# Performance work log

Hardware: AMD Instinct MI355X
Metric: run time of the kernel (lower is better)

## Reference

```python
import jax, jax.numpy as jnp
import numpy as np

B, N, C, H, NC, P = 16, 577, 768, 12, 8, 576  # batch, seq(=patches+cls), dim, heads, curves, patches
D = C // H


def setup_inputs() -> dict:
    key = jax.random.key(0)
    ks = jax.random.split(key, 8)
    x = jax.random.normal(ks[0], (B, N, C), jnp.float32)
    qkv_w = jax.random.normal(ks[1], (C, 3 * C), jnp.float32) * 0.02
    proj_w = jax.random.normal(ks[2], (C, C), jnp.float32) * 0.02
    proj_b = jnp.zeros((C,), jnp.float32)
    # learned per-head decay logits; +3 so sigmoid ~0.95 (slow decay, realistic)
    ai_list = jax.random.normal(ks[3], (NC, H), jnp.float32) + 3.0
    mask_weights = jax.random.normal(ks[4], (NC,), jnp.float32) * 0.1 + 1.0 / NC
    normalize = 1.0 + 0.1 * jax.random.normal(ks[5], (H,), jnp.float32)
    # space-filling-curve inverse index permutations (one per curve)
    curve_inds = jnp.stack([
        jax.random.permutation(jax.random.fold_in(ks[6], c), P) for c in range(NC)
    ]).astype(jnp.int32)
    return dict(x=x, qkv_w=qkv_w, proj_w=proj_w, proj_b=proj_b,
                ai_list=ai_list, mask_weights=mask_weights,
                normalize=normalize, curve_inds=curve_inds)


def _build_mask(ai_list, mask_weights, curve_inds):
    # sigmoid(a)^|i-j| gathered by the curve permutation == sigmoid(a)^|ind_i - ind_j|
    a = jax.nn.sigmoid(ai_list)                                  # [NC,H]
    ci = curve_inds.astype(jnp.float32)                          # [NC,P]
    diff = jnp.abs(ci[:, :, None] - ci[:, None, :])              # [NC,P,P]
    Mc = a[:, :, None, None] ** diff[:, None, :, :]              # [NC,H,P,P]
    Mp = jnp.einsum('c,chpq->hpq', mask_weights, Mc)             # weighted sum over curves
    # cls-token row/col: each curve contributes ones -> sum of weights
    sw = jnp.sum(mask_weights)
    M = jnp.pad(Mp, ((0, 0), (1, 0), (1, 0)))                    # [H,N,N]
    M = M.at[:, 0, :].set(sw)
    M = M.at[:, :, 0].set(sw)
    return M


def reference(x, qkv_w, proj_w, proj_b, ai_list, mask_weights, normalize, curve_inds):
    qkv = (x @ qkv_w).reshape(B, N, 3, H, D)
    q = jnp.transpose(qkv[:, :, 0], (0, 2, 1, 3))                # [B,H,N,D]
    k = jnp.transpose(qkv[:, :, 1], (0, 2, 1, 3))
    v = jnp.transpose(qkv[:, :, 2], (0, 2, 1, 3))
    # NOTE: original overwrites self.scale with the bool `scale`=True -> multiply by 1
    attn = jnp.einsum('bhnd,bhmd->bhnm', q, k)                   # [B,H,N,N]
    M = _build_mask(ai_list, mask_weights, curve_inds)           # [H,N,N]
    attn = attn * M[None] * normalize[None, :, None, None]       # method='mul_v1'
    attn = jax.nn.softmax(attn, axis=-1)
    out = jnp.einsum('bhnm,bhmd->bhnd', attn, v)
    out = jnp.transpose(out, (0, 2, 1, 3)).reshape(B, N, C)
    return out @ proj_w + proj_b
```

## Files before the change

kernel.cpp:

```cpp
#include <hip/hip_runtime.h>


typedef _Float16 f16;
typedef _Float16 half8 __attribute__((ext_vector_type(8)));
typedef _Float16 half4 __attribute__((ext_vector_type(4)));
typedef float floatx4 __attribute__((ext_vector_type(4)));

#define DEVINL __device__ __forceinline__

#define Bb 16
#define NN 577
#define CC 768
#define HH 12
#define DD 64
#define MM (Bb * NN)
#define VTLD 584
#define MLD 580
#define CLD 136
#define TLD 264

DEVINL void async_copy16(void* lds, const void* g) {
  __builtin_amdgcn_global_load_lds(
      (const __attribute__((address_space(1))) void*)g,
      (__attribute__((address_space(3))) void*)lds, 16, 0, 0);
}

DEVINL half8 ld_swz(const f16* lds, int row, int chunk) {
  return *(const half8*)(lds + row * 64 + ((chunk ^ (row & 7)) << 3));
}

DEVINL int xcd_swizzle(int orig, int nwg) {
  int q = nwg >> 3, r = nwg & 7;
  int xcd = orig & 7, loc = orig >> 3;
  return (xcd < r ? xcd * (q + 1) : r * (q + 1) + (xcd - r) * q) + loc;
}

__global__ __launch_bounds__(256)
void prep_kernel(const float* __restrict__ x, const float* __restrict__ qkvw,
                 const float* __restrict__ pw, const float* __restrict__ ai,
                 const float* __restrict__ mw, const float* __restrict__ nrm,
                 const int* __restrict__ ci, f16* __restrict__ x_h,
                 f16* __restrict__ w_t, f16* __restrict__ pw_t,
                 float* __restrict__ Mb) {
  __shared__ float shm[32 * 33];
  const int bid = blockIdx.x;
  const int tid = threadIdx.x;
  if (bid < 6924) {
    int i = (bid * 256 + tid) * 4;
    float4 v = *(const float4*)(x + i);
    half4 o = {(f16)v.x, (f16)v.y, (f16)v.z, (f16)v.w};
    *(half4*)(x_h + i) = o;
  } else if (bid < 9228) {
    bool isq = bid < 8652;
    int b2 = bid - (isq ? 6924 : 8652);
    int N3 = isq ? 3 * CC : CC;
    const float* in = isq ? qkvw : pw;
    f16* out = isq ? w_t : pw_t;
    const int k0 = (b2 % 24) * 32, n0 = (b2 / 24) * 32;
    const int tx = tid & 31, ty = tid >> 5;
#pragma unroll
    for (int p = 0; p < 4; ++p)
      shm[(ty + p * 8) * 33 + tx] = in[(size_t)(k0 + ty + p * 8) * N3 + n0 + tx];
    __syncthreads();
#pragma unroll
    for (int p = 0; p < 4; ++p)
      out[(size_t)(n0 + ty + p * 8) * CC + k0 + tx] = (f16)shm[tx * 33 + ty + p * 8];
  } else {
    int b4 = bid - 9228;
    int i = b4 % NN, h = b4 / NN;
    float* la_s = shm; float* wv_s = shm + 8; float* cif = shm + 16;
    float* swn_s = shm + 24;
    if (tid < 8) {
      float av = ai[tid * 12 + h];
      float a = 1.f / (1.f + __expf(-av));
      la_s[tid] = __logf(a);
      wv_s[tid] = mw[tid];
      cif[tid] = (i > 0) ? (float)ci[tid * 576 + (i - 1)] : 0.f;
    }
    if (tid == 0) {
      float s = 0.f;
      for (int c = 0; c < 8; ++c) s += mw[c];
      swn_s[0] = s * nrm[h] * 1.44269504088896f;
    }
    __syncthreads();
    const float nr = nrm[h] * 1.44269504088896f;
    float* row = Mb + ((size_t)h * NN + i) * MLD;
    for (int j = tid; j < NN; j += 256) {
      float val;
      if (i == 0 || j == 0) {
        val = swn_s[0];
      } else {
        float acc = 0.f;
#pragma unroll
        for (int c = 0; c < 8; ++c) {
          float d = fabsf(cif[c] - (float)ci[c * 576 + (j - 1)]);
          acc += wv_s[c] * __expf(la_s[c] * d);
        }
        val = acc * nr;
      }
      row[j] = val;
    }
  }
}

DEVINL void gemm_mainloop(const f16* __restrict__ A, const f16* __restrict__ Bt,
                          int arow0, int brow0, int maxar,
                          f16* SMEM, floatx4 acc[4][4], int tid) {
  const int lane = tid & 63;
  const int wid = tid >> 6;
  const int wr = wid >> 1, wc = wid & 1;
  const int l15 = lane & 15, g = lane >> 4;
  const int r_ = tid >> 3, cp_ = tid & 7;
  const int lc_ = (cp_ ^ (r_ & 7)) << 3;

  auto stage = [&](f16* As, f16* Bs, int k0) {
#pragma unroll
    for (int q = 0; q < 4; ++q) {
      int r = q * 64 + r_;
      int ar = arow0 + r; if (ar > maxar) ar = maxar;
      async_copy16(As + (q * 512 + tid) * 8, A + (size_t)ar * CC + k0 + lc_);
    }
#pragma unroll
    for (int q = 0; q < 2; ++q) {
      int r = q * 64 + r_;
      async_copy16(Bs + (q * 512 + tid) * 8, Bt + (size_t)(brow0 + r) * CC + k0 + lc_);
    }
  };
  auto compute = [&](const f16* As, const f16* Bs) {
#pragma unroll
    for (int kk = 0; kk < 2; ++kk) {
      half8 af[4], bf[4];
#pragma unroll
      for (int mi = 0; mi < 4; ++mi) af[mi] = ld_swz(As, wr * 64 + mi * 16 + l15, kk * 4 + g);
#pragma unroll
      for (int ni = 0; ni < 4; ++ni) bf[ni] = ld_swz(Bs, wc * 64 + ni * 16 + l15, kk * 4 + g);
#pragma unroll
      for (int mi = 0; mi < 4; ++mi)
#pragma unroll
        for (int ni = 0; ni < 4; ++ni)
          acc[mi][ni] = __builtin_amdgcn_mfma_f32_16x16x32_f16(af[mi], bf[ni], acc[mi][ni], 0, 0, 0);
    }
  };

  const int nt = CC / 64;
  stage(SMEM, SMEM + 16384, 0);
#pragma unroll 1
  for (int t = 0; t < nt; ++t) {
    f16* cAs = (t & 1) ? SMEM + 24576 : SMEM;
    f16* cBs = (t & 1) ? SMEM + 40960 : SMEM + 16384;
    f16* nAs = (t & 1) ? SMEM : SMEM + 24576;
    f16* nBs = (t & 1) ? SMEM + 16384 : SMEM + 40960;
    if (t + 1 < nt) {
      stage(nAs, nBs, (t + 1) * 64);
      asm volatile("s_waitcnt vmcnt(6)" ::: "memory");
    } else {
      asm volatile("s_waitcnt vmcnt(0)" ::: "memory");
    }
    __builtin_amdgcn_s_barrier();
    __builtin_amdgcn_sched_barrier(0);
    compute(cAs, cBs);
    __builtin_amdgcn_s_barrier();
  }
}

__global__ __launch_bounds__(512, 2)
void gemm_qkv(const f16* __restrict__ A, const f16* __restrict__ Bt,
              f16* __restrict__ qb, f16* __restrict__ kb, f16* __restrict__ vt) {
  __shared__ __align__(16) f16 SMEM[49152];
  floatx4 acc[4][4] = {};
  const int nwg = 18 * 37;
  const int wgid = xcd_swizzle(blockIdx.y * gridDim.x + blockIdx.x, nwg);
  const int m0 = (wgid / 18) * 256, n0 = (wgid % 18) * 128;
  gemm_mainloop(A, Bt, m0, n0, MM - 1, SMEM, acc, threadIdx.x);
  const int tid = threadIdx.x, lane = tid & 63, wid = tid >> 6;
  const int wr = wid >> 1, wc = wid & 1, l15 = lane & 15, g = lane >> 4;
  const int t = n0 / CC;
  const int h0 = (n0 - t * CC) >> 6;
  if (t < 2) {
#pragma unroll
    for (int mi = 0; mi < 4; ++mi)
#pragma unroll
      for (int ni = 0; ni < 4; ++ni)
#pragma unroll
        for (int r = 0; r < 4; ++r)
          SMEM[(wr * 64 + mi * 16 + 4 * g + r) * CLD + wc * 64 + ni * 16 + l15] =
              (f16)acc[mi][ni][r];
    __syncthreads();
    f16* dst = (t == 0) ? qb : kb;
#pragma unroll
    for (int p = 0; p < 8; ++p) {
      int c = p * 512 + tid;
      int ml = c >> 4, n3c = (c & 15) << 3;
      int mg = m0 + ml;
      if (mg < MM) {
        int b = mg / NN, n = mg - b * NN;
        int h = h0 + (n3c >> 6), d0 = n3c & 63;
        half8 v = *(const half8*)(SMEM + ml * CLD + n3c);
        *(half8*)(dst + ((size_t)(b * HH + h) * NN + n) * DD + d0) = v;
      }
    }
  } else {
#pragma unroll
    for (int mi = 0; mi < 4; ++mi)
#pragma unroll
      for (int ni = 0; ni < 4; ++ni)
#pragma unroll
        for (int r = 0; r < 4; ++r)
          SMEM[(wc * 64 + ni * 16 + l15) * TLD + wr * 64 + mi * 16 + 4 * g + r] =
              (f16)acc[mi][ni][r];
    __syncthreads();
#pragma unroll
    for (int p = 0; p < 8; ++p) {
      int c = p * 512 + tid;
      int n3 = c >> 5, mc = (c & 31) << 3;
      int mg = m0 + mc;
      int h = h0 + (n3 >> 6), d = n3 & 63;
      half8 v = *(const half8*)(SMEM + n3 * TLD + mc);
      int b0 = mg / NN;
      if (mg + 7 < MM && (mg + 7) / NN == b0) {
        *(half8*)(vt + ((size_t)(b0 * HH + h) * DD + d) * VTLD + (mg - b0 * NN)) = v;
      } else {
#pragma unroll
        for (int e = 0; e < 8; ++e) {
          int m2 = mg + e;
          if (m2 < MM) {
            int b = m2 / NN;
            vt[((size_t)(b * HH + h) * DD + d) * VTLD + (m2 - b * NN)] = v[e];
          }
        }
      }
    }
  }
}

__global__ __launch_bounds__(512, 2)
void gemm_proj(const f16* __restrict__ A, const f16* __restrict__ Bt,
               const float* __restrict__ bias, float* __restrict__ out) {
  __shared__ __align__(16) f16 SMEM[49152];
  floatx4 acc[4][4] = {};
  const int nwg = 6 * 37;
  const int wgid = xcd_swizzle(blockIdx.y * gridDim.x + blockIdx.x, nwg);
  const int m0 = (wgid / 6) * 256, n0 = (wgid % 6) * 128;
  gemm_mainloop(A, Bt, m0, n0, MM - 1, SMEM, acc, threadIdx.x);
  const int lane = threadIdx.x & 63, wid = threadIdx.x >> 6;
  const int wr = wid >> 1, wc = wid & 1, l15 = lane & 15, g = lane >> 4;
#pragma unroll
  for (int mi = 0; mi < 4; ++mi)
#pragma unroll
    for (int ni = 0; ni < 4; ++ni)
#pragma unroll
      for (int r = 0; r < 4; ++r) {
        int m = m0 + wr * 64 + mi * 16 + 4 * g + r;
        if (m >= MM) continue;
        int n = n0 + wc * 64 + ni * 16 + l15;
        out[(size_t)m * CC + n] = acc[mi][ni][r] + bias[n];
      }
}

__global__ __launch_bounds__(512, 4)
void attn_kernel(const f16* __restrict__ qb, const f16* __restrict__ kb,
                 const f16* __restrict__ vt, const float* __restrict__ Mb,
                 f16* __restrict__ aout) {
  __shared__ f16 Ks[2][64 * 64];
  __shared__ f16 Vs[2][64 * 64];
  const int D0 = (blockIdx.z * gridDim.y + blockIdx.y) * gridDim.x + blockIdx.x;
  const int wgid = xcd_swizzle(D0, 5 * HH * Bb);
  const int it = wgid % 5;
  const int rem = wgid / 5;
  const int b = rem % Bb, h = rem / Bb;
  const int tid = threadIdx.x, lane = tid & 63, wid = tid >> 6;
  const int l15 = lane & 15, g = lane >> 4;
  const size_t bh = (size_t)b * HH + h;
  const f16* qbh = qb + bh * NN * DD;
  const f16* kbh = kb + bh * NN * DD;
  const f16* vbh = vt + bh * DD * VTLD;
  const float* Mh = Mb + (size_t)h * NN * MLD;
  const int row0w = it * 128 + wid * 16;

  half8 qB0, qB1;
  {
    int qr = row0w + l15; if (qr > NN - 1) qr = NN - 1;
    const f16* qp = qbh + (size_t)qr * DD + g * 8;
    qB0 = *(const half8*)qp;
    qB1 = *(const half8*)(qp + 32);
  }
  const float* Mrow;
  {
    int r0 = row0w + l15; if (r0 > NN - 1) r0 = NN - 1;
    Mrow = Mh + (size_t)r0 * MLD + 4 * g;
  }

  floatx4 acc[4] = {};
  float lsum = 0.f;
  float mrun = -3e38f;

  const int sr_ = tid >> 3, scp_ = tid & 7;
  const int slc_ = (scp_ ^ (sr_ & 7)) << 3;
  auto stage = [&](f16* Kd, f16* Vd, int j0) {
    int j = j0 + sr_; if (j > NN - 1) j = NN - 1;
    async_copy16(Kd + tid * 8, kbh + (size_t)j * DD + slc_);
    async_copy16(Vd + tid * 8, vbh + (size_t)sr_ * VTLD + j0 + slc_);
  };
  auto ldmask = [&](floatx4 m4[4], int j0) {
#pragma unroll
    for (int jt = 0; jt < 4; ++jt)
      m4[jt] = *(const floatx4*)(Mrow + j0 + jt * 16);
  };
  auto compute = [&](const f16* Kc, const f16* Vc, floatx4 m4[4], int j0) {
    floatx4 sf[4];
#pragma unroll
    for (int jt = 0; jt < 4; ++jt) {
      half8 ka0 = ld_swz(Kc, jt * 16 + l15, g);
      half8 ka1 = ld_swz(Kc, jt * 16 + l15, 4 + g);
      floatx4 z = {0.f, 0.f, 0.f, 0.f};
      z = __builtin_amdgcn_mfma_f32_16x16x32_f16(ka0, qB0, z, 0, 0, 0);
      z = __builtin_amdgcn_mfma_f32_16x16x32_f16(ka1, qB1, z, 0, 0, 0);
      sf[jt] = z;
    }
#pragma unroll
    for (int jt = 0; jt < 4; ++jt)
#pragma unroll
      for (int r = 0; r < 4; ++r) sf[jt][r] *= m4[jt][r];
    if (j0 + 64 > NN) {
#pragma unroll
      for (int jt = 0; jt < 4; ++jt)
#pragma unroll
        for (int r = 0; r < 4; ++r)
          if (j0 + jt * 16 + 4 * g + r >= NN) sf[jt][r] = -3e38f;
    }
    float pj[4];
#pragma unroll
    for (int jt = 0; jt < 4; ++jt)
      pj[jt] = fmaxf(fmaxf(sf[jt][0], sf[jt][1]), fmaxf(sf[jt][2], sf[jt][3]));
    float pmax = fmaxf(fmaxf(pj[0], pj[1]), fmaxf(pj[2], pj[3]));
    pmax = fmaxf(pmax, __shfl_xor(pmax, 16));
    pmax = fmaxf(pmax, __shfl_xor(pmax, 32));
    if (!__all(pmax - mrun <= 8.f)) {
      float mnew = fmaxf(mrun, pmax);
      float fac = __builtin_amdgcn_exp2f(mrun - mnew);
      mrun = mnew;
      lsum *= fac;
#pragma unroll
      for (int dt = 0; dt < 4; ++dt)
#pragma unroll
        for (int r = 0; r < 4; ++r) acc[dt][r] *= fac;
    }
    half4 pB[4];
    float lsj[4];
#pragma unroll
    for (int jt = 0; jt < 4; ++jt) {
      half4 pb;
      float p0 = __builtin_amdgcn_exp2f(sf[jt][0] - mrun);
      float p1 = __builtin_amdgcn_exp2f(sf[jt][1] - mrun);
      float p2 = __builtin_amdgcn_exp2f(sf[jt][2] - mrun);
      float p3 = __builtin_amdgcn_exp2f(sf[jt][3] - mrun);
      pb[0] = (f16)p0; pb[1] = (f16)p1; pb[2] = (f16)p2; pb[3] = (f16)p3;
      lsj[jt] = (p0 + p1) + (p2 + p3);
      pB[jt] = pb;
    }
    lsum += (lsj[0] + lsj[1]) + (lsj[2] + lsj[3]);
#pragma unroll
    for (int dt = 0; dt < 4; ++dt)
#pragma unroll
      for (int jt = 0; jt < 4; ++jt) {
        int c16 = (jt * 2 + (g >> 1)) ^ (l15 & 7);
        half4 va = *(const half4*)(Vc + (dt * 16 + l15) * 64 + (c16 << 3) + (g & 1) * 4);
        acc[dt] = __builtin_amdgcn_mfma_f32_16x16x16f16(va, pB[jt], acc[dt], 0, 0, 0);
      }
  };

  floatx4 m4A[4], m4B[4];
  stage(Ks[0], Vs[0], 0);
  ldmask(m4A, 0);

#pragma unroll 1
  for (int t = 0; t < 10; t += 2) {
    ldmask(m4B, (t + 1) * 64);
    asm volatile("s_waitcnt vmcnt(4)" ::: "memory");
    __builtin_amdgcn_s_barrier();
    __builtin_amdgcn_sched_barrier(0);
    stage(Ks[1], Vs[1], (t + 1) * 64);
    compute(Ks[0], Vs[0], m4A, t * 64);
    const int j2 = (t + 2 < 10) ? (t + 2) * 64 : 0;
    ldmask(m4A, j2);
    asm volatile("s_waitcnt vmcnt(4)" ::: "memory");
    __builtin_amdgcn_s_barrier();
    __builtin_amdgcn_sched_barrier(0);
    stage(Ks[0], Vs[0], j2);
    compute(Ks[1], Vs[1], m4B, (t + 1) * 64);
  }

  {
    float v = lsum;
    v += __shfl_xor(v, 16);
    v += __shfl_xor(v, 32);
    float linv = 1.f / v;
    int n = row0w + l15;
    if (n < NN) {
#pragma unroll
      for (int dt = 0; dt < 4; ++dt) {
        half4 o;
#pragma unroll
        for (int r = 0; r < 4; ++r) o[r] = (f16)(acc[dt][r] * linv);
        *(half4*)(aout + ((size_t)(b * NN + n)) * CC + h * DD + dt * 16 + 4 * g) = o;
      }
    }
  }
}

extern "C" void kernel_launch(void* const* d_in, const int* in_sizes, int n_in,
                              void* d_out, int out_size, void* d_ws, size_t ws_size,
                              hipStream_t stream) {
  const float* x    = (const float*)d_in[0];
  const float* qkvw = (const float*)d_in[1];
  const float* pw   = (const float*)d_in[2];
  const float* pb   = (const float*)d_in[3];
  const float* ai   = (const float*)d_in[4];
  const float* mw   = (const float*)d_in[5];
  const float* nrm  = (const float*)d_in[6];
  const int*   ci   = (const int*)d_in[7];
  float* out = (float*)d_out;

  char* wsb = (char*)d_ws;
  size_t off = 0;
  auto alloc = [&](size_t bytes) {
    char* p = wsb + off;
    off += (bytes + 255) & ~(size_t)255;
    return p;
  };
  f16*   x_h  = (f16*)alloc((size_t)MM * CC * 2);
  f16*   w_t  = (f16*)alloc((size_t)3 * CC * CC * 2);
  f16*   pw_t = (f16*)alloc((size_t)CC * CC * 2);
  float* Mb   = (float*)alloc((size_t)HH * NN * MLD * 4 + 1024);
  f16*   qb   = (f16*)alloc((size_t)Bb * HH * NN * DD * 2);
  f16*   kb   = (f16*)alloc((size_t)Bb * HH * NN * DD * 2);
  f16*   vt   = (f16*)alloc((size_t)Bb * HH * DD * VTLD * 2);
  (void)alloc(4096);
  f16* aout = x_h;

  prep_kernel<<<16152, 256, 0, stream>>>(x, qkvw, pw, ai, mw, nrm, ci,
                                         x_h, w_t, pw_t, Mb);
  gemm_qkv<<<dim3(18, 37), 512, 0, stream>>>(x_h, w_t, qb, kb, vt);
  attn_kernel<<<dim3(5, HH, Bb), 512, 0, stream>>>(qb, kb, vt, Mb, aout);
  gemm_proj<<<dim3(6, 37), 512, 0, stream>>>(aout, pw_t, pb, out);
}
```

Baseline: 150.3 us.

## Permute V tile during async staging so PV reads use 16-byte LDS loads

Replaces the single 16-byte async copy of each V row chunk with four 4-byte async copies that scatter V elements into a permuted LDS layout. The layout is chosen so each lane can fetch its PV operands with two swizzled half8 loads per d-tile instead of four half4 loads. It also moves the cross-lane max shuffles inside the rescale branch so they run only when the running max must change. The trade is four times as many, smaller global-to-LDS transactions per V tile, which may cost more in memory-instruction issue than the LDS reads save.

```diff
diff --git a/kernel.cpp b/kernel.cpp
--- a/kernel.cpp
+++ b/kernel.cpp
@@ -23,6 +23,11 @@
   __builtin_amdgcn_global_load_lds(
       (const __attribute__((address_space(1))) void*)g,
       (__attribute__((address_space(3))) void*)lds, 16, 0, 0);
+}
+DEVINL void async_copy4(void* lds, const void* g) {
+  __builtin_amdgcn_global_load_lds(
+      (const __attribute__((address_space(1))) void*)g,
+      (__attribute__((address_space(3))) void*)lds, 4, 0, 0);
 }
 
 DEVINL half8 ld_swz(const f16* lds, int row, int chunk) {
@@ -296,10 +301,24 @@
 
   const int sr_ = tid >> 3, scp_ = tid & 7;
   const int slc_ = (scp_ ^ (sr_ & 7)) << 3;
+  int vsj[4], vsd[4];
+#pragma unroll
+  for (int q = 0; q < 4; ++q) {
+    int G = q * 512 + tid;
+    int d = G >> 5;
+    int cs = (G >> 2) & 7, g4 = G & 3;
+    int o4 = ((cs ^ (d & 7)) << 2) | g4;
+    int c = o4 >> 2;
+    vsj[q] = ((c & 1) << 5) | ((o4 & 2) << 3) | ((c >> 1) << 2) | ((o4 & 1) << 1);
+    vsd[q] = d;
+  }
   auto stage = [&](f16* Kd, f16* Vd, int j0) {
     int j = j0 + sr_; if (j > NN - 1) j = NN - 1;
     async_copy16(Kd + tid * 8, kbh + (size_t)j * DD + slc_);
-    async_copy16(Vd + tid * 8, vbh + (size_t)sr_ * VTLD + j0 + slc_);
+#pragma unroll
+    for (int q = 0; q < 4; ++q)
+      async_copy4(Vd + (q * 512 + tid) * 2,
+                  vbh + (size_t)vsd[q] * VTLD + j0 + vsj[q]);
   };
   auto ldmask = [&](floatx4 m4[4], int j0) {
 #pragma unroll
@@ -332,10 +351,10 @@
 #pragma unroll
     for (int jt = 0; jt < 4; ++jt)
       pj[jt] = fmaxf(fmaxf(sf[jt][0], sf[jt][1]), fmaxf(sf[jt][2], sf[jt][3]));
-    float pmax = fmaxf(fmaxf(pj[0], pj[1]), fmaxf(pj[2], pj[3]));
-    pmax = fmaxf(pmax, __shfl_xor(pmax, 16));
-    pmax = fmaxf(pmax, __shfl_xor(pmax, 32));
-    if (!__all(pmax - mrun <= 8.f)) {
+    float pmax_loc = fmaxf(fmaxf(pj[0], pj[1]), fmaxf(pj[2], pj[3]));
+    if (__any(pmax_loc - mrun > 8.f)) {
+      float pmax = fmaxf(pmax_loc, __shfl_xor(pmax_loc, 16));
+      pmax = fmaxf(pmax, __shfl_xor(pmax, 32));
       float mnew = fmaxf(mrun, pmax);
       float fac = __builtin_amdgcn_exp2f(mrun - mnew);
       mrun = mnew;
@@ -360,13 +379,18 @@
     }
     lsum += (lsj[0] + lsj[1]) + (lsj[2] + lsj[3]);
 #pragma unroll
-    for (int dt = 0; dt < 4; ++dt)
-#pragma unroll
-      for (int jt = 0; jt < 4; ++jt) {
-        int c16 = (jt * 2 + (g >> 1)) ^ (l15 & 7);
-        half4 va = *(const half4*)(Vc + (dt * 16 + l15) * 64 + (c16 << 3) + (g & 1) * 4);
-        acc[dt] = __builtin_amdgcn_mfma_f32_16x16x16f16(va, pB[jt], acc[dt], 0, 0, 0);
-      }
+    for (int dt = 0; dt < 4; ++dt) {
+      half8 v0 = ld_swz(Vc, dt * 16 + l15, 2 * g);
+      half8 v1 = ld_swz(Vc, dt * 16 + l15, 2 * g + 1);
+      half4 a0 = __builtin_shufflevector(v0, v0, 0, 1, 2, 3);
+      half4 a1 = __builtin_shufflevector(v0, v0, 4, 5, 6, 7);
+      half4 a2 = __builtin_shufflevector(v1, v1, 0, 1, 2, 3);
+      half4 a3 = __builtin_shufflevector(v1, v1, 4, 5, 6, 7);
+      acc[dt] = __builtin_amdgcn_mfma_f32_16x16x16f16(a0, pB[0], acc[dt], 0, 0, 0);
+      acc[dt] = __builtin_amdgcn_mfma_f32_16x16x16f16(a1, pB[1], acc[dt], 0, 0, 0);
+      acc[dt] = __builtin_amdgcn_mfma_f32_16x16x16f16(a2, pB[2], acc[dt], 0, 0, 0);
+      acc[dt] = __builtin_amdgcn_mfma_f32_16x16x16f16(a3, pB[3], acc[dt], 0, 0, 0);
+    }
   };
 
   floatx4 m4A[4], m4B[4];
```

Measured after the change: 154.2 us. 1.03x slower.
